# Performance work log

Hardware: AMD Instinct MI355X
Metric: run time of the kernel (lower is better)

The kernel has to match this reference:

```python
import jax, jax.numpy as jnp
import numpy as np

K = 20          # neighbour_num
EMB = 512       # emb_dims
EPS = 1e-12     # guards sqrt grad at self-neighbor zero distance


def setup_inputs() -> dict:
    key = jax.random.key(0)
    ks = jax.random.split(key, 6)
    B, D, N = 8, 3, 4096
    C_in = 2 * D + K  # 26 = 6 + neighbour_num
    def xavier(k, o, c):
        return jax.random.normal(k, (o, c), jnp.float32) * jnp.sqrt(2.0 / (o + c))
    return {
        "x":  jax.random.normal(ks[0], (B, D, N), jnp.float32),
        "w1": xavier(ks[1], 64, C_in),
        "w2": xavier(ks[2], 64, 64),
        "w3": xavier(ks[3], 128, 64),
        "w4": xavier(ks[4], 256, 128),
        "w5": xavier(ks[5], EMB, 512),
    }


def _graph_feature(x):
    # x: (B, D, N). Returns (B, 2D+K, N, K).
    B, D, N = x.shape
    xt = jnp.swapaxes(x, 1, 2)                      # (B, N, D)
    sq = jnp.sum(x * x, axis=1)                     # (B, N)
    # pairwise = -||xi - xj||^2 ; topk picks nearest neighbors (incl. self)
    pair = 2.0 * jnp.einsum('bdn,bdm->bnm', x, x) - sq[:, :, None] - sq[:, None, :]
    idx = jax.lax.top_k(pair, K)[1]                 # (B, N, K) int32
    nbr = xt[jnp.arange(B)[:, None, None], idx]     # (B, N, K, D) gather
    xc = jnp.broadcast_to(xt[:, :, None, :], (B, N, K, D))
    dist = jnp.sqrt(jnp.sum((nbr - xc) ** 2, axis=-1) + EPS)   # (B, N, K)
    distr = jnp.broadcast_to(dist[:, :, None, :], (B, N, K, K))
    feat = jnp.concatenate([xc, nbr, distr], axis=-1)          # (B, N, K, 2D+K)
    return jnp.transpose(feat, (0, 3, 1, 2))        # (B, 2D+K, N, K)


def _conv1x1(h, w):
    # h: (B, C, N, K), w: (O, C)  -> (B, O, N, K)
    return jnp.einsum('bcnk,oc->bonk', h, w)


def reference(x, w1, w2, w3, w4, w5):
    h = _graph_feature(x)                           # (B, 26, N, K)
    h = jax.nn.relu(_conv1x1(h, w1)); x1 = h.max(axis=-1)   # (B, 64, N)
    h = jax.nn.relu(_conv1x1(h, w2)); x2 = h.max(axis=-1)   # (B, 64, N)
    h = jax.nn.relu(_conv1x1(h, w3)); x3 = h.max(axis=-1)   # (B, 128, N)
    h = jax.nn.relu(_conv1x1(h, w4)); x4 = h.max(axis=-1)   # (B, 256, N)
    cat = jnp.concatenate([x1, x2, x3, x4], axis=1)          # (B, 512, N)
    out = jax.nn.relu(jnp.einsum('bcn,oc->bon', cat, w5))    # (B, EMB, N)
    return out
```

## Files before the change

### kernel.cpp

```cpp
#include <hip/hip_runtime.h>
#include <cstdint>
#include <cstddef>

#define NB   8
#define NPTS 4096
#define KNN  20
#define P    4
#define QPW  4

typedef __attribute__((ext_vector_type(8))) short    short8;
typedef __attribute__((ext_vector_type(4))) float    floatx4;
typedef __attribute__((ext_vector_type(2))) uint32_t uint2v;

__device__ __forceinline__ uint16_t f2bf(float f) {
    uint32_t u = __float_as_uint(f);
    uint32_t r = (u + 0x7FFFu + ((u >> 16) & 1u)) >> 16;
    return (uint16_t)r;
}

__device__ __forceinline__ uint32_t cvtpk_bf16(float lo, float hi) {
    uint32_t r;
    asm("v_cvt_pk_bf16_f32 %0, %1, %2" : "=v"(r) : "v"(lo), "v"(hi));
    return r;
}

__device__ __forceinline__ uint32_t max2u16(uint32_t a, uint32_t b) {
    const uint32_t al = a & 0xFFFFu, ah = a >> 16;
    const uint32_t bl = b & 0xFFFFu, bh = b >> 16;
    const uint32_t l = al > bl ? al : bl;
    const uint32_t h = ah > bh ? ah : bh;
    return l | (h << 16);
}

__device__ __forceinline__ uint32_t umin32(uint32_t a, uint32_t b) { return a < b ? a : b; }
__device__ __forceinline__ uint32_t umax32(uint32_t a, uint32_t b) { return a > b ? a : b; }

template <int CTRL>
__device__ __forceinline__ uint32_t dpp_maxu(uint32_t v) {
    uint32_t o = (uint32_t)__builtin_amdgcn_update_dpp((int)v, (int)v,
                                                       CTRL, 0xF, 0xF, false);
    return umax32(v, o);
}
__device__ __forceinline__ uint32_t wave_max_u32(uint32_t v) {
    v = dpp_maxu<0x111>(v);
    v = dpp_maxu<0x112>(v);
    v = dpp_maxu<0x114>(v);
    v = dpp_maxu<0x118>(v);
    v = dpp_maxu<0x142>(v);
    v = dpp_maxu<0x143>(v);
    return (uint32_t)__builtin_amdgcn_readlane((int)v, 63);
}

__global__ __launch_bounds__(256) void topk_kernel(
    const float4* __restrict__ xyzs,
    int*   __restrict__ idx_out,
    float* __restrict__ dist_out)
{
    const int t = threadIdx.x;
    const int wave = t >> 6, l = t & 63;
    const int nbase = (blockIdx.x * 4 + wave) * QPW;
    const int b = blockIdx.y;
    const float4* xq = xyzs + (size_t)b * NPTS;

    float xn0[QPW], xn1[QPW], xn2[QPW], sqn[QPW];
    uint32_t V0[QPW], V1[QPW], V2[QPW];
    unsigned long long consumed[QPW];
    int my_m[QPW];

    #pragma unroll
    for (int p = 0; p < QPW; ++p) {
        const float4 pn = xq[nbase + p];
        xn0[p] = pn.x; xn1[p] = pn.y; xn2[p] = pn.z; sqn[p] = pn.w;
        V0[p] = 0u; V1[p] = 0u; V2[p] = 0u;
        consumed[p] = 0ull;
        my_m[p] = 0;
    }

    #pragma unroll 4
    for (int j = 0; j < 64; ++j) {
        const float4 pm = xq[j * 64 + l];
        const uint32_t jx = (uint32_t)(j ^ 63);
        #pragma unroll
        for (int p = 0; p < QPW; ++p) {
            const float dot = fmaf(xn2[p], pm.z, fmaf(xn1[p], pm.y, xn0[p] * pm.x));
            const float s = fmaf(2.0f, dot, -sqn[p]) - pm.w;
            const uint32_t key = (~__float_as_uint(s) & 0xFFFFFFC0u) | jx;
            const uint32_t t1 = umin32(V0[p], key);
            const uint32_t t2 = umin32(V1[p], key);
            V0[p] = umax32(V0[p], key);
            V1[p] = umax32(V1[p], t1);
            V2[p] = umax32(V2[p], t2);
        }
    }

    #pragma unroll
    for (int p = 0; p < QPW; ++p) {
        for (int k = 0; k < KNN; ++k) {
            if (V0[p] == 0u) {
                V1[p] = 0u; V2[p] = 0u;
                for (int j = 0; j < 64; ++j) {
                    const float4 pm = xq[j * 64 + l];
                    const float dot = fmaf(xn2[p], pm.z, fmaf(xn1[p], pm.y, xn0[p] * pm.x));
                    const float s = fmaf(2.0f, dot, -sqn[p]) - pm.w;
                    uint32_t key = (~__float_as_uint(s) & 0xFFFFFFC0u)
                                 | (uint32_t)(j ^ 63);
                    if ((consumed[p] >> j) & 1ull) key = 0u;
                    const uint32_t t1 = umin32(V0[p], key);
                    const uint32_t t2 = umin32(V1[p], key);
                    V0[p] = umax32(V0[p], key);
                    V1[p] = umax32(V1[p], t1);
                    V2[p] = umax32(V2[p], t2);
                }
            }
            const uint32_t w = wave_max_u32(V0[p]);
            const unsigned long long own = __ballot(V0[p] == w);
            const int owner = (int)__builtin_ctzll(own);
            const int jwin  = 63 - (int)(w & 63u);
            const int m     = jwin * 64 + owner;
            if (l == k) my_m[p] = m;
            if (l == owner) {
                consumed[p] |= 1ull << jwin;
                V0[p] = V1[p]; V1[p] = V2[p]; V2[p] = 0u;
            }
        }
    }

    #pragma unroll
    for (int p = 0; p < QPW; ++p) {
        if (l < KNN) {
            const int n = nbase + p;
            const float4 pm = xq[my_m[p]];
            const float d0 = pm.x - xn0[p], d1 = pm.y - xn1[p], d2 = pm.z - xn2[p];
            const float dist = sqrtf(((d0 * d0 + d1 * d1) + d2 * d2) + 1e-12f);
            const size_t base = ((size_t)b * NPTS + n) * KNN + l;
            idx_out[base]  = my_m[p];
            dist_out[base] = dist;
        }
    }
}

__global__ __launch_bounds__(256) void prep_all(
    const float* __restrict__ x,
    const float* __restrict__ w1, const float* __restrict__ w2,
    const float* __restrict__ w3, const float* __restrict__ w4,
    const float* __restrict__ w5,
    uint16_t* __restrict__ wf1, uint16_t* __restrict__ wf2,
    uint16_t* __restrict__ wf3, uint16_t* __restrict__ wf4,
    uint16_t* __restrict__ w5b,
    float4* __restrict__ xyzs)
{
    int blk = blockIdx.x;
    const int t = threadIdx.x;
    if (blk < 1024) {
        const int i = blk * 256 + t;
        w5b[i] = f2bf(w5[i]);
        return;
    }
    blk -= 1024;
    if (blk >= 23) {
        const int i = (blk - 23) * 256 + t;
        if (i < NB * NPTS) {
            const int b = i / NPTS, n = i - b * NPTS;
            const float* xb = x + (size_t)b * 3 * NPTS;
            const float x0 = xb[n], x1 = xb[NPTS + n], x2 = xb[2 * NPTS + n];
            float4 v;
            v.x = x0; v.y = x1; v.z = x2;
            v.w = fmaf(x2, x2, fmaf(x1, x1, x0 * x0));
            xyzs[i] = v;
        }
        return;
    }
    const float* w; uint16_t* frag; int C, NT, KT, base;
    if (blk < 1)       { w = w1; frag = wf1; C = 26;  NT = 4;  KT = 1; base = blk; }
    else if (blk < 3)  { w = w2; frag = wf2; C = 64;  NT = 4;  KT = 2; base = blk - 1; }
    else if (blk < 7)  { w = w3; frag = wf3; C = 64;  NT = 8;  KT = 2; base = blk - 3; }
    else               { w = w4; frag = wf4; C = 128; NT = 16; KT = 4; base = blk - 7; }
    const int i = base * 256 + t;
    if (i >= NT * KT * 64) return;
    const int lane = i & 63;
    const int kt   = (i >> 6) % KT;
    const int nt   = (i >> 6) / KT;
    const int n    = nt * 16 + (lane & 15);
    const int c0   = kt * 32 + (lane >> 4) * 8;
    uint16_t o[8];
    #pragma unroll
    for (int j = 0; j < 8; ++j) {
        const int c = c0 + j;
        o[j] = (c < C) ? f2bf(w[(size_t)n * C + c]) : (uint16_t)0;
    }
    uint16_t* dst = frag + (size_t)i * 8;
    #pragma unroll
    for (int j = 0; j < 8; ++j) dst[j] = o[j];
}

template <int NT_TOT, int KT, int IN_STRIDE, int OUT_STRIDE>
__device__ __forceinline__ void mfma_layer(const uint16_t* __restrict__ in,
                                           uint16_t* __restrict__ out,
                                           const uint16_t* __restrict__ wf,
                                           int wave, int lane) {
    constexpr int NT_W = NT_TOT / 4;
    const int col = lane & 15, quad = lane >> 4;
    short8 bfrag[NT_W][KT];
    #pragma unroll
    for (int ni = 0; ni < NT_W; ++ni)
        #pragma unroll
        for (int k = 0; k < KT; ++k)
            bfrag[ni][k] = *(const short8*)(wf +
                ((size_t)((wave * NT_W + ni) * KT + k) * 64 + lane) * 8);
    #pragma unroll
    for (int mt = 0; mt < 5; ++mt) {
        short8 af[KT];
        #pragma unroll
        for (int k = 0; k < KT; ++k)
            af[k] = *(const short8*)(in + (mt * 16 + col) * IN_STRIDE + k * 32 + quad * 8);
        #pragma unroll
        for (int ni = 0; ni < NT_W; ++ni) {
            floatx4 acc = {0.f, 0.f, 0.f, 0.f};
            #pragma unroll
            for (int k = 0; k < KT; ++k)
                acc = __builtin_amdgcn_mfma_f32_16x16x32_bf16(bfrag[ni][k], af[k], acc, 0, 0, 0);
            const int nt = wave * NT_W + ni;
            const uint32_t pk01 = cvtpk_bf16(fmaxf(acc[0], 0.f), fmaxf(acc[1], 0.f));
            const uint32_t pk23 = cvtpk_bf16(fmaxf(acc[2], 0.f), fmaxf(acc[3], 0.f));
            uint2v pk; pk.x = pk01; pk.y = pk23;
            *(uint2v*)(out + (mt * 16 + col) * OUT_STRIDE + nt * 16 + quad * 4) = pk;
        }
    }
}

template <int O, int STRIDE>
__device__ __forceinline__ void maxk(const uint16_t* __restrict__ h,
                                     uint16_t* __restrict__ cat_ws, int catoff,
                                     int t, int b, int n0) {
    constexpr int G = O / 8;
    if (t < P * G) {
        const int p = t / G, g = t % G;
        uint16_t mx[8];
        #pragma unroll
        for (int j = 0; j < 8; ++j) mx[j] = 0;
        for (int k = 0; k < KNN; ++k) {
            const uint16_t* row = h + (p * KNN + k) * STRIDE + g * 8;
            #pragma unroll
            for (int j = 0; j < 8; ++j) mx[j] = row[j] > mx[j] ? row[j] : mx[j];
        }
        uint16_t* dst = cat_ws + ((size_t)b * NPTS + n0 + p) * 512 + catoff + g * 8;
        *(short8*)dst = *(const short8*)mx;
    }
}

__global__ __launch_bounds__(256) void fused_mlp_mfma(
    const float* __restrict__ x,
    const int*   __restrict__ idx_ws,
    const float* __restrict__ dist_ws,
    const uint16_t* __restrict__ wf1,
    const uint16_t* __restrict__ wf2,
    const uint16_t* __restrict__ wf3,
    const uint16_t* __restrict__ wf4,
    uint16_t* __restrict__ cat_ws)
{
    const int n0 = blockIdx.x * P, b = blockIdx.y, t = threadIdx.x;
    const int wave = t >> 6, lane = t & 63;

    __shared__ __align__(16) uint16_t bufA[6400];
    __shared__ __align__(16) uint16_t bufB[10880];

    for (int i = t; i < 1600; i += 256) ((uint32_t*)bufA)[i] = 0;
    __syncthreads();
    {
        const float* xb = x + (size_t)b * 3 * NPTS;
        if (t < P * KNN) {
            const int p = t / KNN, k = t % KNN;
            const int n = n0 + p;
            const size_t base = ((size_t)b * NPTS + n) * KNN + k;
            const int   m = idx_ws[base];
            const float d = dist_ws[base];
            uint16_t* fr = bufA + t * 40;
            fr[0] = f2bf(xb[n]);        fr[1] = f2bf(xb[NPTS + n]);
            fr[2] = f2bf(xb[2 * NPTS + n]);
            fr[3] = f2bf(xb[m]);        fr[4] = f2bf(xb[NPTS + m]);
            fr[5] = f2bf(xb[2 * NPTS + m]);
            const uint16_t db = f2bf(d);
            #pragma unroll
            for (int j = 0; j < KNN; ++j) bufA[(p * KNN + j) * 40 + 6 + k] = db;
        }
    }
    __syncthreads();

    mfma_layer<4, 1, 40, 72>(bufA, bufB, wf1, wave, lane);
    __syncthreads();

    maxk<64, 72>(bufB, cat_ws, 0, t, b, n0);
    mfma_layer<4, 2, 72, 72>(bufB, bufA, wf2, wave, lane);
    __syncthreads();

    maxk<64, 72>(bufA, cat_ws, 64, t, b, n0);
    mfma_layer<8, 2, 72, 136>(bufA, bufB, wf3, wave, lane);
    __syncthreads();

    maxk<128, 136>(bufB, cat_ws, 128, t, b, n0);
    {
        uint16_t* slab = bufA + wave * 1600;
        const int col = lane & 15, quad = lane >> 4;
        #pragma unroll
        for (int ni = 0; ni < 4; ++ni) {
            const int nt = wave * 4 + ni;
            short8 bfrag[4];
            #pragma unroll
            for (int k = 0; k < 4; ++k)
                bfrag[k] = *(const short8*)(wf4 + ((size_t)(nt * 4 + k) * 64 + lane) * 8);
            #pragma unroll
            for (int mt = 0; mt < 5; ++mt) {
                floatx4 acc = {0.f, 0.f, 0.f, 0.f};
                #pragma unroll
                for (int k = 0; k < 4; ++k) {
                    const short8 af = *(const short8*)(bufB + (mt * 16 + col) * 136
                                                           + k * 32 + quad * 8);
                    acc = __builtin_amdgcn_mfma_f32_16x16x32_bf16(bfrag[k], af, acc, 0, 0, 0);
                }
                uint2v pk;
                pk.x = cvtpk_bf16(fmaxf(acc[0], 0.f), fmaxf(acc[1], 0.f));
                pk.y = cvtpk_bf16(fmaxf(acc[2], 0.f), fmaxf(acc[3], 0.f));
                *(uint2v*)&slab[(mt * 16 + col) * 20 + quad * 4] = pk;
            }
            const int p = lane >> 4, grp = (lane >> 2) & 3, kq = lane & 3;
            uint32_t m01 = 0u, m23 = 0u;
            #pragma unroll
            for (int i = 0; i < 5; ++i) {
                const uint2v v = *(const uint2v*)&slab[(p * KNN + kq * 5 + i) * 20 + grp * 4];
                m01 = max2u16(m01, v.x);
                m23 = max2u16(m23, v.y);
            }
            m01 = max2u16(m01, (uint32_t)__shfl_xor((int)m01, 1));
            m23 = max2u16(m23, (uint32_t)__shfl_xor((int)m23, 1));
            m01 = max2u16(m01, (uint32_t)__shfl_xor((int)m01, 2));
            m23 = max2u16(m23, (uint32_t)__shfl_xor((int)m23, 2));
            if (kq == 0) {
                uint32_t* dst = (uint32_t*)(cat_ws + ((size_t)b * NPTS + n0 + p) * 512
                              + 256 + nt * 16 + grp * 4);
                dst[0] = m01; dst[1] = m23;
            }
        }
    }
}

__global__ __launch_bounds__(256) void final_gemm_mfma(
    const uint16_t* __restrict__ w5b,
    const uint16_t* __restrict__ cat,
    float* __restrict__ out)
{
    const int b  = blockIdx.z;
    const int o0 = blockIdx.y * 64;
    const int n0 = blockIdx.x * 128;
    const int t  = threadIdx.x;
    const int wave = t >> 6, lane = t & 63;
    const int col = lane & 15, quad = lane >> 4;

    __shared__ __align__(16) uint16_t As[64 * 72];
    __shared__ __align__(16) uint16_t Bs[128 * 72];

    floatx4 acc[8];
    #pragma unroll
    for (int i = 0; i < 8; ++i) acc[i] = (floatx4){0.f, 0.f, 0.f, 0.f};

    const size_t arow_base = (size_t)o0 * 512;
    const size_t brow_base = ((size_t)b * NPTS + n0) * 512;

    for (int kc = 0; kc < 512; kc += 64) {
        #pragma unroll
        for (int i = 0; i < 2; ++i) {
            const int idx = t + i * 256;
            const int row = idx >> 3;
            const int k8  = (idx & 7) * 8;
            *(short8*)&As[row * 72 + k8] =
                *(const short8*)&w5b[arow_base + (size_t)row * 512 + kc + k8];
        }
        #pragma unroll
        for (int i = 0; i < 4; ++i) {
            const int idx = t + i * 256;
            const int row = idx >> 3;
            const int k8  = (idx & 7) * 8;
            *(short8*)&Bs[row * 72 + k8] =
                *(const short8*)&cat[brow_base + (size_t)row * 512 + kc + k8];
        }
        __syncthreads();
        #pragma unroll
        for (int kt = 0; kt < 2; ++kt) {
            const short8 af = *(const short8*)&As[(wave * 16 + col) * 72 + kt * 32 + quad * 8];
            #pragma unroll
            for (int ns = 0; ns < 8; ++ns) {
                const short8 bf = *(const short8*)&Bs[(ns * 16 + col) * 72 + kt * 32 + quad * 8];
                acc[ns] = __builtin_amdgcn_mfma_f32_16x16x32_bf16(af, bf, acc[ns], 0, 0, 0);
            }
        }
        __syncthreads();
    }

    #pragma unroll
    for (int ns = 0; ns < 8; ++ns) {
        #pragma unroll
        for (int r = 0; r < 4; ++r) {
            out[((size_t)b * 512 + o0 + wave * 16 + quad * 4 + r) * NPTS
                + n0 + ns * 16 + col] = fmaxf(acc[ns][r], 0.f);
        }
    }
}

extern "C" void kernel_launch(void* const* d_in, const int* in_sizes, int n_in,
                              void* d_out, int out_size, void* d_ws, size_t ws_size,
                              hipStream_t stream) {
    const float* x  = (const float*)d_in[0];
    const float* w1 = (const float*)d_in[1];
    const float* w2 = (const float*)d_in[2];
    const float* w3 = (const float*)d_in[3];
    const float* w4 = (const float*)d_in[4];
    const float* w5 = (const float*)d_in[5];
    float* out = (float*)d_out;

    char* ws = (char*)d_ws;
    int*      idx_ws  = (int*)ws;
    float*    dist_ws = (float*)(ws + 2621440);
    uint16_t* cat_ws  = (uint16_t*)(ws + 5242880);
    float4*   xyzs    = (float4*)(ws + 5242880);
    uint16_t* w5b     = (uint16_t*)(ws + 38797312);
    uint16_t* wf1     = (uint16_t*)(ws + 72351744);
    uint16_t* wf2     = (uint16_t*)(ws + 72351744 + 4096);
    uint16_t* wf3     = (uint16_t*)(ws + 72351744 + 4096 + 8192);
    uint16_t* wf4     = (uint16_t*)(ws + 72351744 + 4096 + 8192 + 16384);

    prep_all<<<dim3(1024 + 23 + 128), 256, 0, stream>>>(
        x, w1, w2, w3, w4, w5, wf1, wf2, wf3, wf4, w5b, xyzs);

    topk_kernel<<<dim3(NPTS / (4 * QPW), NB), 256, 0, stream>>>(xyzs, idx_ws, dist_ws);
    fused_mlp_mfma<<<dim3(NPTS / P, NB), 256, 0, stream>>>(
        x, idx_ws, dist_ws, wf1, wf2, wf3, wf4, cat_ws);
    final_gemm_mfma<<<dim3(NPTS / 128, 512 / 64, NB), 256, 0, stream>>>(w5b, cat_ws, out);
}
```

Baseline: 306.5 us.

## Swizzle layer-3 LDS layout, shrink LDS buffers, enlarge final GEMM output tile

Layer 3's activations are now stored with an XOR swizzle at a 128-element stride instead of 136 padding, and the layer-4 max slab stride drops from 20 to 18. Together these cut shared memory per block, which may let more blocks run per CU in the fused MLP kernel, while trying to keep bank conflicts low. The final GEMM now computes 128 output channels per block instead of 64, so each loaded cat tile is reused twice and half as many blocks are launched. The trade-off is more accumulator registers per thread and odd-stride 32-bit stores into the slab.

```diff
diff --git a/kernel.cpp b/kernel.cpp
--- a/kernel.cpp
+++ b/kernel.cpp
@@ -193,7 +193,7 @@
     for (int j = 0; j < 8; ++j) dst[j] = o[j];
 }
 
-template <int NT_TOT, int KT, int IN_STRIDE, int OUT_STRIDE>
+template <int NT_TOT, int KT, int IN_STRIDE, int OUT_STRIDE, int SWZO>
 __device__ __forceinline__ void mfma_layer(const uint16_t* __restrict__ in,
                                            uint16_t* __restrict__ out,
                                            const uint16_t* __restrict__ wf,
@@ -223,12 +223,14 @@
             const uint32_t pk01 = cvtpk_bf16(fmaxf(acc[0], 0.f), fmaxf(acc[1], 0.f));
             const uint32_t pk23 = cvtpk_bf16(fmaxf(acc[2], 0.f), fmaxf(acc[3], 0.f));
             uint2v pk; pk.x = pk01; pk.y = pk23;
-            *(uint2v*)(out + (mt * 16 + col) * OUT_STRIDE + nt * 16 + quad * 4) = pk;
-        }
-    }
-}
-
-template <int O, int STRIDE>
+            int oc = nt * 16 + quad * 4;
+            if (SWZO) oc ^= (col & 7) << 3;
+            *(uint2v*)(out + (mt * 16 + col) * OUT_STRIDE + oc) = pk;
+        }
+    }
+}
+
+template <int O, int STRIDE, int SWZ>
 __device__ __forceinline__ void maxk(const uint16_t* __restrict__ h,
                                      uint16_t* __restrict__ cat_ws, int catoff,
                                      int t, int b, int n0) {
@@ -239,9 +241,11 @@
         #pragma unroll
         for (int j = 0; j < 8; ++j) mx[j] = 0;
         for (int k = 0; k < KNN; ++k) {
-            const uint16_t* row = h + (p * KNN + k) * STRIDE + g * 8;
-            #pragma unroll
-            for (int j = 0; j < 8; ++j) mx[j] = row[j] > mx[j] ? row[j] : mx[j];
+            const int row = p * KNN + k;
+            const int c = SWZ ? ((g * 8) ^ ((row & 7) << 3)) : g * 8;
+            const uint16_t* rp = h + row * STRIDE + c;
+            #pragma unroll
+            for (int j = 0; j < 8; ++j) mx[j] = rp[j] > mx[j] ? rp[j] : mx[j];
         }
         uint16_t* dst = cat_ws + ((size_t)b * NPTS + n0 + p) * 512 + catoff + g * 8;
         *(short8*)dst = *(const short8*)mx;
@@ -261,8 +265,8 @@
     const int n0 = blockIdx.x * P, b = blockIdx.y, t = threadIdx.x;
     const int wave = t >> 6, lane = t & 63;
 
-    __shared__ __align__(16) uint16_t bufA[6400];
-    __shared__ __align__(16) uint16_t bufB[10880];
+    __shared__ __align__(16) uint16_t bufA[5760];
+    __shared__ __align__(16) uint16_t bufB[10240];
 
     for (int i = t; i < 1600; i += 256) ((uint32_t*)bufA)[i] = 0;
     __syncthreads();
@@ -286,20 +290,20 @@
     }
     __syncthreads();
 
-    mfma_layer<4, 1, 40, 72>(bufA, bufB, wf1, wave, lane);
+    mfma_layer<4, 1, 40, 72, 0>(bufA, bufB, wf1, wave, lane);
     __syncthreads();
 
-    maxk<64, 72>(bufB, cat_ws, 0, t, b, n0);
-    mfma_layer<4, 2, 72, 72>(bufB, bufA, wf2, wave, lane);
+    maxk<64, 72, 0>(bufB, cat_ws, 0, t, b, n0);
+    mfma_layer<4, 2, 72, 72, 0>(bufB, bufA, wf2, wave, lane);
     __syncthreads();
 
-    maxk<64, 72>(bufA, cat_ws, 64, t, b, n0);
-    mfma_layer<8, 2, 72, 136>(bufA, bufB, wf3, wave, lane);
+    maxk<64, 72, 0>(bufA, cat_ws, 64, t, b, n0);
+    mfma_layer<8, 2, 72, 128, 1>(bufA, bufB, wf3, wave, lane);
     __syncthreads();
 
-    maxk<128, 136>(bufB, cat_ws, 128, t, b, n0);
+    maxk<128, 128, 1>(bufB, cat_ws, 128, t, b, n0);
     {
-        uint16_t* slab = bufA + wave * 1600;
+        uint16_t* slab = bufA + wave * 1440;
         const int col = lane & 15, quad = lane >> 4;
         #pragma unroll
         for (int ni = 0; ni < 4; ++ni) {
@@ -310,25 +314,26 @@
                 bfrag[k] = *(const short8*)(wf4 + ((size_t)(nt * 4 + k) * 64 + lane) * 8);
             #pragma unroll
             for (int mt = 0; mt < 5; ++mt) {
+                const int row = mt * 16 + col;
                 floatx4 acc = {0.f, 0.f, 0.f, 0.f};
                 #pragma unroll
                 for (int k = 0; k < 4; ++k) {
-                    const short8 af = *(const short8*)(bufB + (mt * 16 + col) * 136
-                                                           + k * 32 + quad * 8);
+                    const short8 af = *(const short8*)(bufB + row * 128
+                                        + ((k * 32 + quad * 8) ^ ((col & 7) << 3)));
                     acc = __builtin_amdgcn_mfma_f32_16x16x32_bf16(bfrag[k], af, acc, 0, 0, 0);
                 }
-                uint2v pk;
-                pk.x = cvtpk_bf16(fmaxf(acc[0], 0.f), fmaxf(acc[1], 0.f));
-                pk.y = cvtpk_bf16(fmaxf(acc[2], 0.f), fmaxf(acc[3], 0.f));
-                *(uint2v*)&slab[(mt * 16 + col) * 20 + quad * 4] = pk;
+                uint32_t* sp = (uint32_t*)&slab[row * 18 + quad * 4];
+                sp[0] = cvtpk_bf16(fmaxf(acc[0], 0.f), fmaxf(acc[1], 0.f));
+                sp[1] = cvtpk_bf16(fmaxf(acc[2], 0.f), fmaxf(acc[3], 0.f));
             }
             const int p = lane >> 4, grp = (lane >> 2) & 3, kq = lane & 3;
             uint32_t m01 = 0u, m23 = 0u;
             #pragma unroll
             for (int i = 0; i < 5; ++i) {
-                const uint2v v = *(const uint2v*)&slab[(p * KNN + kq * 5 + i) * 20 + grp * 4];
-                m01 = max2u16(m01, v.x);
-                m23 = max2u16(m23, v.y);
+                const uint32_t* rp = (const uint32_t*)
+                    &slab[(p * KNN + kq * 5 + i) * 18 + grp * 4];
+                m01 = max2u16(m01, rp[0]);
+                m23 = max2u16(m23, rp[1]);
             }
             m01 = max2u16(m01, (uint32_t)__shfl_xor((int)m01, 1));
             m23 = max2u16(m23, (uint32_t)__shfl_xor((int)m23, 1));
@@ -349,25 +354,27 @@
     float* __restrict__ out)
 {
     const int b  = blockIdx.z;
-    const int o0 = blockIdx.y * 64;
+    const int o0 = blockIdx.y * 128;
     const int n0 = blockIdx.x * 128;
     const int t  = threadIdx.x;
     const int wave = t >> 6, lane = t & 63;
     const int col = lane & 15, quad = lane >> 4;
 
-    __shared__ __align__(16) uint16_t As[64 * 72];
+    __shared__ __align__(16) uint16_t As[128 * 72];
     __shared__ __align__(16) uint16_t Bs[128 * 72];
 
-    floatx4 acc[8];
-    #pragma unroll
-    for (int i = 0; i < 8; ++i) acc[i] = (floatx4){0.f, 0.f, 0.f, 0.f};
+    floatx4 acc[2][8];
+    #pragma unroll
+    for (int i = 0; i < 2; ++i)
+        #pragma unroll
+        for (int j = 0; j < 8; ++j) acc[i][j] = (floatx4){0.f, 0.f, 0.f, 0.f};
 
     const size_t arow_base = (size_t)o0 * 512;
     const size_t brow_base = ((size_t)b * NPTS + n0) * 512;
 
     for (int kc = 0; kc < 512; kc += 64) {
         #pragma unroll
-        for (int i = 0; i < 2; ++i) {
+        for (int i = 0; i < 4; ++i) {
             const int idx = t + i * 256;
             const int row = idx >> 3;
             const int k8  = (idx & 7) * 8;
@@ -385,22 +392,33 @@
         __syncthreads();
         #pragma unroll
         for (int kt = 0; kt < 2; ++kt) {
-            const short8 af = *(const short8*)&As[(wave * 16 + col) * 72 + kt * 32 + quad * 8];
+            short8 af[2];
+            #pragma unroll
+            for (int os = 0; os < 2; ++os)
+                af[os] = *(const short8*)&As[(wave * 32 + os * 16 + col) * 72
+                                             + kt * 32 + quad * 8];
             #pragma unroll
             for (int ns = 0; ns < 8; ++ns) {
-                const short8 bf = *(const short8*)&Bs[(ns * 16 + col) * 72 + kt * 32 + quad * 8];
-                acc[ns] = __builtin_amdgcn_mfma_f32_16x16x32_bf16(af, bf, acc[ns], 0, 0, 0);
+                const short8 bf = *(const short8*)&Bs[(ns * 16 + col) * 72
+                                                      + kt * 32 + quad * 8];
+                #pragma unroll
+                for (int os = 0; os < 2; ++os)
+                    acc[os][ns] = __builtin_amdgcn_mfma_f32_16x16x32_bf16(
+                        af[os], bf, acc[os][ns], 0, 0, 0);
             }
         }
         __syncthreads();
     }
 
     #pragma unroll
-    for (int ns = 0; ns < 8; ++ns) {
-        #pragma unroll
-        for (int r = 0; r < 4; ++r) {
-            out[((size_t)b * 512 + o0 + wave * 16 + quad * 4 + r) * NPTS
-                + n0 + ns * 16 + col] = fmaxf(acc[ns][r], 0.f);
+    for (int os = 0; os < 2; ++os) {
+        #pragma unroll
+        for (int ns = 0; ns < 8; ++ns) {
+            #pragma unroll
+            for (int r = 0; r < 4; ++r) {
+                out[((size_t)b * 512 + o0 + wave * 32 + os * 16 + quad * 4 + r) * NPTS
+                    + n0 + ns * 16 + col] = fmaxf(acc[os][ns][r], 0.f);
+            }
         }
     }
 }
@@ -433,5 +451,5 @@
     topk_kernel<<<dim3(NPTS / (4 * QPW), NB), 256, 0, stream>>>(xyzs, idx_ws, dist_ws);
     fused_mlp_mfma<<<dim3(NPTS / P, NB), 256, 0, stream>>>(
         x, idx_ws, dist_ws, wf1, wf2, wf3, wf4, cat_ws);
-    final_gemm_mfma<<<dim3(NPTS / 128, 512 / 64, NB), 256, 0, stream>>>(w5b, cat_ws, out);
-}
+    final_gemm_mfma<<<dim3(NPTS / 128, 512 / 128, NB), 256, 0, stream>>>(w5b, cat_ws, out);
+}
```

Result: no change. 302.9 us (-1.2%).
